# Optimization experiments

Hardware: AMD Instinct MI355X
Metric: run time of the kernel (lower is better)

## Reference

```python
import jax, jax.numpy as jnp
import numpy as np

N, E, NNZ = 50000, 10000, 250000   # nodes, hyperedges, incidences
IN_CH, H, D = 128, 64, 6           # in_channels, MLP_hidden, stalk dim
EPS = 1e-5


def setup_inputs() -> dict:
    key = jax.random.key(0)
    ks = jax.random.split(key, 12)
    inp = {}
    inp["x"] = jax.random.normal(ks[0], (N, IN_CH), jnp.float32)
    inp["hyperedge_attr"] = jax.random.normal(ks[1], (E, IN_CH), jnp.float32)  # init_hedge='rand'
    inp["node_idx"] = jax.random.randint(ks[2], (NNZ,), 0, N)
    inp["edge_idx"] = jax.random.randint(ks[3], (NNZ,), 0, E)
    inp["node_types"] = jax.random.randint(ks[4], (N,), 0, 3)
    inp["hyperedge_types"] = jax.random.randint(ks[5], (E,), 0, 6)
    s = 1.0 / np.sqrt(IN_CH)
    inp["W_lin"] = jax.random.uniform(ks[6], (IN_CH, H * D), jnp.float32, -s, s)
    inp["b_lin"] = jnp.zeros((H * D,), jnp.float32)
    inp["ln_g"] = jnp.ones((2 * H,), jnp.float32)
    inp["ln_b"] = jnp.zeros((2 * H,), jnp.float32)
    s2 = 1.0 / np.sqrt(2 * H)
    inp["W_sheaf"] = jax.random.uniform(ks[7], (2 * H, D), jnp.float32, -s2, s2)
    inp["b_sheaf"] = jnp.zeros((D,), jnp.float32)
    s3 = 1.0 / np.sqrt(H)
    inp["W_conv0"] = jax.random.uniform(ks[8], (H, H), jnp.float32, -s3, s3)
    inp["b_conv0"] = jnp.zeros((H,), jnp.float32)
    inp["W_conv1"] = jax.random.uniform(ks[9], (H, H), jnp.float32, -s3, s3)
    inp["b_conv1"] = jnp.zeros((H,), jnp.float32)
    return inp


def _layernorm(x, g, b):
    mu = x.mean(-1, keepdims=True)
    var = ((x - mu) ** 2).mean(-1, keepdims=True)
    return (x - mu) * jax.lax.rsqrt(var + EPS) * g + b


def reference(x, hyperedge_attr, node_idx, edge_idx, node_types, hyperedge_types,
              W_lin, b_lin, ln_g, ln_b, W_sheaf, b_sheaf,
              W_conv0, b_conv0, W_conv1, b_conv1):
    # --- input projection + stalk reshape (self.lin) ---
    xs = (x @ W_lin + b_lin).reshape(N * D, H)              # [N*d, H]
    es = (hyperedge_attr @ W_lin + b_lin).reshape(E * D, H)  # [E*d, H]

    # --- SheafBuilderDiag (local_concat, sigmoid act) ---
    xa = xs.reshape(N, D, H).mean(1)   # [N, H] stalk-averaged node feats
    ea = es.reshape(E, D, H).mean(1)   # [E, H]
    feat = jnp.concatenate([xa[node_idx], ea[edge_idx]], axis=-1)  # [NNZ, 2H]
    alpha = jax.nn.sigmoid(_layernorm(feat, ln_g, ln_b) @ W_sheaf + b_sheaf)  # [NNZ, D]

    dr = jnp.arange(D)
    row_exp = (node_idx[:, None] * D + dr).reshape(-1)  # [NNZ*D] expanded node index
    col_exp = (edge_idx[:, None] * D + dr).reshape(-1)  # [NNZ*D] expanded hyperedge index
    a = alpha.reshape(-1)                               # [NNZ*D]

    # --- degree_norm: D^-1 (nodes) and B^-1 (hyperedges) from incidence counts ---
    ones = jnp.ones_like(a)
    Dn = jax.ops.segment_sum(ones, row_exp, num_segments=N * D)
    Dinv = jnp.where(Dn > 0, 1.0 / Dn, 0.0)
    Bn = jax.ops.segment_sum(ones, col_exp, num_segments=E * D)
    Binv = jnp.where(Bn > 0, 1.0 / Bn, 0.0)

    def conv(xin, W, bias):
        # HyperDiffusionDiagSheafConv: out = xW - D^-1 H^T B^-1 H (xW) + bias
        xl = xin @ W
        m = Binv[:, None] * jax.ops.segment_sum(a[:, None] * xl[row_exp], col_exp, num_segments=E * D)
        agg = Dinv[:, None] * jax.ops.segment_sum(a[:, None] * m[col_exp], row_exp, num_segments=N * D)
        return xl - agg + bias

    h1 = jax.nn.elu(conv(xs, W_conv0, b_conv0))   # dropout inactive (eval)
    h2 = conv(h1, W_conv1, b_conv1)
    return jax.nn.elu(h2.reshape(N, H * D))
```

## Files before the change

### kernel.cpp

```cpp
#include <hip/hip_runtime.h>
#include <hip/hip_bf16.h>

#define N_NODES 50000
#define N_EDGES 10000
#define NNZV    250000
#define IN_CH   128
#define HDIM    64
#define DSTALK  6
#define HD      384
#define NROWS   (N_NODES * DSTALK)
#define EROWS   (N_EDGES * DSTALK)

__global__ __launch_bounds__(256) void k_wefft(
    const float* __restrict__ W_lin, const float* __restrict__ W0,
    float* __restrict__ W0effT) {
  int idx = blockIdx.x * blockDim.x + threadIdx.x;
  if (idx >= IN_CH * HD) return;
  int k = idx / HD, j = idx - k * HD;
  int r = j >> 6, h = j & 63;
  float s = 0.f;
#pragma unroll 8
  for (int m = 0; m < HDIM; m++)
    s += W_lin[k * HD + r * HDIM + m] * W0[m * HDIM + h];
  W0effT[(size_t)j * IN_CH + k] = s;
}

#define WS_BASE (IN_CH * HDIM + HD + HDIM)
#define WS_END  (WS_BASE + 780 + HDIM * HDIM)
__global__ __launch_bounds__(256) void k_wsmall(
    const float* __restrict__ W_lin, const float* __restrict__ b_lin,
    const float* __restrict__ W0, const float* __restrict__ W1,
    const float* __restrict__ g, const float* __restrict__ bln,
    const float* __restrict__ Ws, const float* __restrict__ bs,
    float* __restrict__ Wm, float* __restrict__ cm, float* __restrict__ c0,
    float* __restrict__ gwN, float* __restrict__ gwE,
    float* __restrict__ G, float* __restrict__ K, float* __restrict__ W1T) {
  int idx = blockIdx.x * blockDim.x + threadIdx.x;
  if (idx < IN_CH * HDIM) {
    int k = idx >> 6, h = idx & 63;
    float s = 0.f;
#pragma unroll
    for (int r = 0; r < DSTALK; r++) s += W_lin[k * HD + r * HDIM + h];
    Wm[idx] = s * (1.f / 6.f);
  } else if (idx < IN_CH * HDIM + HD) {
    int j = idx - IN_CH * HDIM;
    int r = j >> 6, h = j & 63;
    float s = 0.f;
#pragma unroll 8
    for (int m = 0; m < HDIM; m++) s += b_lin[r * HDIM + m] * W0[m * HDIM + h];
    c0[j] = s;
  } else if (idx < WS_BASE) {
    int h = idx - IN_CH * HDIM - HD;
    float s = 0.f;
#pragma unroll
    for (int r = 0; r < DSTALK; r++) s += b_lin[r * HDIM + h];
    cm[h] = s * (1.f / 6.f);
  } else if (idx < WS_BASE + 384) {
    int i = idx - WS_BASE;
    int h = i / 6, r = i - h * 6;
    gwN[i] = g[h] * Ws[h * DSTALK + r];
  } else if (idx < WS_BASE + 768) {
    int i = idx - WS_BASE - 384;
    int h = i / 6, r = i - h * 6;
    gwE[i] = g[64 + h] * Ws[(64 + h) * DSTALK + r];
  } else if (idx < WS_BASE + 774) {
    int r = idx - WS_BASE - 768;
    float s = 0.f;
    for (int i = 0; i < 2 * HDIM; i++) s += g[i] * Ws[i * DSTALK + r];
    G[r] = s;
  } else if (idx < WS_BASE + 780) {
    int r = idx - WS_BASE - 774;
    float s = 0.f;
    for (int i = 0; i < 2 * HDIM; i++) s += bln[i] * Ws[i * DSTALK + r];
    K[r] = s + bs[r];
  } else if (idx < WS_END) {
    int i = idx - WS_BASE - 780;
    int c = i >> 6, k = i & 63;
    W1T[c * HDIM + k] = W1[k * HDIM + c];
  }
}

__global__ __launch_bounds__(256) void k_xa_stats(
    const float* __restrict__ x, const float* __restrict__ ea,
    const float* __restrict__ Wm, const float* __restrict__ cm,
    const float* __restrict__ gwN, const float* __restrict__ gwE,
    float* __restrict__ stats) {
  __shared__ float lx[64][IN_CH];
  __shared__ float ox[64][HDIM + 1];
  __shared__ float lgw[2][64 * DSTALK];
  const int row0 = blockIdx.x * 64;
  const int tid = threadIdx.x;
  for (int i = tid; i < 2 * 64 * DSTALK; i += 256) {
    int which = i / 384, k = i - which * 384;
    lgw[which][k] = which ? gwE[k] : gwN[k];
  }
  for (int i = tid; i < 64 * IN_CH; i += 256) {
    int r = i >> 7, k = i & 127;
    int row = row0 + r;
    float v = 0.f;
    if (row < N_NODES) v = x[row * IN_CH + k];
    else if (row < N_NODES + N_EDGES) v = ea[(row - N_NODES) * IN_CH + k];
    lx[r][k] = v;
  }
  __syncthreads();
  const int col = tid & 63, rg = tid >> 6;
  float acc[16];
#pragma unroll
  for (int i = 0; i < 16; i++) acc[i] = 0.f;
  for (int k = 0; k < IN_CH; k++) {
    float w = Wm[k * HDIM + col];
#pragma unroll
    for (int i = 0; i < 16; i++) acc[i] += lx[rg * 16 + i][k] * w;
  }
  const float c = cm[col];
#pragma unroll
  for (int i = 0; i < 16; i++) ox[rg * 16 + i][col] = acc[i] + c;
  __syncthreads();
  for (int t = tid; t < 512; t += 256) {
    int row = t >> 3, st = t & 7;
    int grow = row0 + row;
    if (grow >= N_NODES + N_EDGES) continue;
    const float* __restrict__ gw = (grow >= N_NODES) ? lgw[1] : lgw[0];
    float s = 0.f;
    if (st == 0) {
#pragma unroll 8
      for (int h = 0; h < HDIM; h++) s += ox[row][h];
    } else if (st == 1) {
#pragma unroll 8
      for (int h = 0; h < HDIM; h++) { float v = ox[row][h]; s += v * v; }
    } else {
      int r = st - 2;
#pragma unroll 8
      for (int h = 0; h < HDIM; h++) s += ox[row][h] * gw[h * DSTALK + r];
    }
    stats[(size_t)grow * 8 + st] = s;
  }
}

__global__ __launch_bounds__(256, 2) void k_xl0(
    const float* __restrict__ x, const float* __restrict__ W0effT,
    const float* __restrict__ c0, float* __restrict__ xl0) {
  __shared__ float4 aS[8][129];
  __shared__ float4 bS[8][129];
  const int tid = threadIdx.x;
  const int row0 = blockIdx.x * 128;
  const int col0 = blockIdx.y * 128;
  const int tc = tid & 15, tr = tid >> 4;
  float acc[8][8];
#pragma unroll
  for (int i = 0; i < 8; i++)
#pragma unroll
    for (int j = 0; j < 8; j++) acc[i][j] = 0.f;

#pragma unroll 1
  for (int kc = 0; kc < 4; kc++) {
    if (kc) __syncthreads();
#pragma unroll
    for (int i = 0; i < 4; i++) {
      int fidx = tid + (i << 8);
      int kq = fidx & 7, row = fidx >> 3;
      int gk = kc * 32 + kq * 4;
      int grow = row0 + row;
      aS[kq][row] = (grow < N_NODES)
                        ? *(const float4*)(x + (size_t)grow * IN_CH + gk)
                        : make_float4(0.f, 0.f, 0.f, 0.f);
    }
#pragma unroll
    for (int i = 0; i < 4; i++) {
      int fidx = tid + (i << 8);
      int kq = fidx & 7, col = fidx >> 3;
      int gk = kc * 32 + kq * 4;
      bS[kq][col] =
          *(const float4*)(W0effT + (size_t)(col0 + col) * IN_CH + gk);
    }
    __syncthreads();
#pragma unroll 1
    for (int kq = 0; kq < 8; kq++) {
      float4 b[8];
#pragma unroll
      for (int j = 0; j < 8; j++) b[j] = bS[kq][tc + (j << 4)];
#pragma unroll
      for (int i = 0; i < 8; i++) {
        float4 a = aS[kq][tr + (i << 4)];
#pragma unroll
        for (int j = 0; j < 8; j++)
          acc[i][j] += a.x * b[j].x + a.y * b[j].y + a.z * b[j].z + a.w * b[j].w;
      }
    }
  }

  float cc[8];
#pragma unroll
  for (int j = 0; j < 8; j++) cc[j] = c0[col0 + tc + (j << 4)];
#pragma unroll
  for (int i = 0; i < 8; i++) {
    int row = row0 + tr + (i << 4);
    if (row >= N_NODES) continue;
    float* __restrict__ orow = xl0 + (size_t)row * HD + col0;
#pragma unroll
    for (int j = 0; j < 8; j++) {
      orow[tc + (j << 4)] = acc[i][j] + cc[j];
    }
  }
}

__global__ __launch_bounds__(256) void k_xw(
    const float* __restrict__ xin, const float* __restrict__ W1T,
    float* __restrict__ xl) {
  __shared__ float4 aS[8][129];
  __shared__ float4 bS[8][65];
  const int tid = threadIdx.x;
  const int row0 = blockIdx.x * 128;
  const int tc = tid & 15, tr = tid >> 4;
  float acc[8][4];
#pragma unroll
  for (int i = 0; i < 8; i++)
#pragma unroll
    for (int j = 0; j < 4; j++) acc[i][j] = 0.f;

#pragma unroll 1
  for (int kc = 0; kc < 2; kc++) {
    if (kc) __syncthreads();
#pragma unroll
    for (int i = 0; i < 4; i++) {
      int fidx = tid + (i << 8);
      int kq = fidx & 7, row = fidx >> 3;
      int gk = kc * 32 + kq * 4;
      int grow = row0 + row;
      aS[kq][row] = (grow < NROWS)
                        ? *(const float4*)(xin + (size_t)grow * HDIM + gk)
                        : make_float4(0.f, 0.f, 0.f, 0.f);
    }
#pragma unroll
    for (int i = 0; i < 2; i++) {
      int fidx = tid + (i << 8);
      int kq = fidx & 7, col = fidx >> 3;
      int gk = kc * 32 + kq * 4;
      bS[kq][col] = *(const float4*)(W1T + col * HDIM + gk);
    }
    __syncthreads();
#pragma unroll 1
    for (int kq = 0; kq < 8; kq++) {
      float4 b[4];
#pragma unroll
      for (int j = 0; j < 4; j++) b[j] = bS[kq][tc + (j << 4)];
#pragma unroll
      for (int i = 0; i < 8; i++) {
        float4 a = aS[kq][tr + (i << 4)];
#pragma unroll
        for (int j = 0; j < 4; j++)
          acc[i][j] += a.x * b[j].x + a.y * b[j].y + a.z * b[j].z + a.w * b[j].w;
      }
    }
  }
#pragma unroll
  for (int i = 0; i < 8; i++) {
    int row = row0 + tr + (i << 4);
    if (row >= NROWS) continue;
#pragma unroll
    for (int j = 0; j < 4; j++) {
      int col = tc + (j << 4);
      xl[(size_t)row * HDIM + col] = acc[i][j];
    }
  }
}

__global__ __launch_bounds__(256) void k_sheaf2(
    const int* __restrict__ nidx, const int* __restrict__ eidx,
    const float* __restrict__ stats,
    const float* __restrict__ G, const float* __restrict__ K,
    float* __restrict__ alpha) {
  int j = blockIdx.x * blockDim.x + threadIdx.x;
  if (j >= NNZV) return;
  int n = nidx[j], e = eidx[j];
  const float4* __restrict__ sn = (const float4*)(stats + (size_t)n * 8);
  const float4* __restrict__ se = (const float4*)(stats + ((size_t)(N_NODES + e)) * 8);
  float4 a0 = sn[0], a1 = sn[1];
  float4 b0 = se[0], b1 = se[1];
  float mu = (a0.x + b0.x) * (1.f / 128.f);
  float var = (a0.y + b0.y) * (1.f / 128.f) - mu * mu;
  float rs = rsqrtf(var + 1e-5f);
  float p[DSTALK] = {a0.z + b0.z, a0.w + b0.w, a1.x + b1.x,
                     a1.y + b1.y, a1.z + b1.z, a1.w + b1.w};
#pragma unroll
  for (int r = 0; r < DSTALK; r++) {
    float z = rs * (p[r] - mu * G[r]) + K[r];
    alpha[(size_t)j * DSTALK + r] = 1.f / (1.f + expf(-z));
  }
}

__global__ void k_count(const int* __restrict__ nidx, const int* __restrict__ eidx,
                        int* __restrict__ cntN, int* __restrict__ cntE) {
  int j = blockIdx.x * blockDim.x + threadIdx.x;
  if (j < NNZV) {
    atomicAdd(&cntN[nidx[j]], 1);
    atomicAdd(&cntE[eidx[j]], 1);
  }
}

__global__ __launch_bounds__(256) void k_scan_a(
    const int* __restrict__ cnt, int n, int* __restrict__ row,
    int* __restrict__ bsum) {
  const int b = blockIdx.x, t = threadIdx.x;
  const int i0 = b * 512 + 2 * t, i1 = i0 + 1;
  int c0 = (i0 < n) ? cnt[i0] : 0;
  int c1 = (i1 < n) ? cnt[i1] : 0;
  int ts = c0 + c1;
  const int lane = t & 63, wv = t >> 6;
  int s = ts;
#pragma unroll
  for (int o = 1; o < 64; o <<= 1) {
    int v = __shfl_up(s, o);
    if (lane >= o) s += v;
  }
  __shared__ int wsum[4];
  if (lane == 63) wsum[wv] = s;
  __syncthreads();
  int wbase = 0;
#pragma unroll
  for (int wprev = 0; wprev < 3; wprev++)
    if (wprev < wv) wbase += wsum[wprev];
  const int incl = wbase + s;
  const int excl = incl - ts;
  if (i0 < n) row[i0] = excl;
  if (i1 < n) row[i1] = excl + c0;
  if (t == 255) bsum[b] = incl;
}

__global__ __launch_bounds__(128) void k_scan_b(
    const int* __restrict__ bsum, int nb, int* __restrict__ bbase) {
  const int t = threadIdx.x;
  int v = (t < nb) ? bsum[t] : 0;
  const int lane = t & 63, wv = t >> 6;
  int s = v;
#pragma unroll
  for (int o = 1; o < 64; o <<= 1) {
    int u = __shfl_up(s, o);
    if (lane >= o) s += u;
  }
  __shared__ int wsum[2];
  if (lane == 63) wsum[wv] = s;
  __syncthreads();
  const int incl = ((wv == 1) ? wsum[0] : 0) + s;
  if (t < nb) bbase[t] = incl - v;
  if (t == 127) bbase[nb] = incl;
}

__global__ __launch_bounds__(256) void k_scan_c(
    const int* __restrict__ cnt, const int* __restrict__ bbase, int n, int nb,
    int* __restrict__ row, int* __restrict__ fill, float* __restrict__ inv) {
  int i = blockIdx.x * blockDim.x + threadIdx.x;
  if (i < n) {
    int v = row[i] + bbase[i >> 9];
    row[i] = v;
    fill[i] = v;
    int c = cnt[i];
    inv[i] = c > 0 ? 1.f / (float)c : 0.f;
  }
  if (i == 0) row[n] = bbase[nb];
}

__global__ void k_fill(const int* __restrict__ nidx, const int* __restrict__ eidx,
                       int* __restrict__ fillN, int* __restrict__ fillE,
                       int* __restrict__ jlN, int* __restrict__ jlE,
                       int* __restrict__ elN, int* __restrict__ nlE) {
  int j = blockIdx.x * blockDim.x + threadIdx.x;
  if (j < NNZV) {
    int n = nidx[j], e = eidx[j];
    int p = atomicAdd(&fillN[n], 1);
    jlN[p] = j; elN[p] = e;
    int q = atomicAdd(&fillE[e], 1);
    jlE[q] = j; nlE[q] = n;
  }
}

__global__ __launch_bounds__(256) void k_gather_e(
    const int* __restrict__ rowE, const int* __restrict__ jlE,
    const int* __restrict__ nlE, const float* __restrict__ alpha,
    const float* __restrict__ xl, const float* __restrict__ Binv,
    float* __restrict__ msum) {
  int e = (blockIdx.x * blockDim.x + threadIdx.x) >> 6;
  int lane = threadIdx.x & 63;
  if (e >= N_EDGES) return;
  float acc[DSTALK];
#pragma unroll
  for (int r = 0; r < DSTALK; r++) acc[r] = 0.f;
  const int lo = rowE[e], hi = rowE[e + 1];
  int p = lo;
  for (; p + 3 < hi; p += 4) {
    int jj[4], nn[4];
#pragma unroll
    for (int u = 0; u < 4; u++) { jj[u] = jlE[p + u]; nn[u] = nlE[p + u]; }
    float v[4][DSTALK], a[4][DSTALK];
#pragma unroll
    for (int u = 0; u < 4; u++) {
      const float* __restrict__ xr = xl + (size_t)nn[u] * HD + lane;
      const float* __restrict__ ar = alpha + (size_t)jj[u] * DSTALK;
#pragma unroll
      for (int r = 0; r < DSTALK; r++) { v[u][r] = xr[r * HDIM]; a[u][r] = ar[r]; }
    }
#pragma unroll
    for (int r = 0; r < DSTALK; r++)
      acc[r] += a[0][r] * v[0][r] + a[1][r] * v[1][r] +
                a[2][r] * v[2][r] + a[3][r] * v[3][r];
  }
  for (; p < hi; p++) {
    const int j0 = jlE[p], n0 = nlE[p];
    const float* __restrict__ xr0 = xl + (size_t)n0 * HD + lane;
    const float* __restrict__ ar0 = alpha + (size_t)j0 * DSTALK;
#pragma unroll
    for (int r = 0; r < DSTALK; r++) acc[r] += ar0[r] * xr0[r * HDIM];
  }
  const float bv = Binv[e];
  float* __restrict__ mr = msum + (size_t)e * HD + lane;
#pragma unroll
  for (int r = 0; r < DSTALK; r++) mr[r * HDIM] = acc[r] * bv;
}

__global__ __launch_bounds__(256) void k_gather_n(
    const int* __restrict__ rowN, const int* __restrict__ jlN,
    const int* __restrict__ elN, const float* __restrict__ alpha,
    const float* __restrict__ msum, const float* __restrict__ Dinv,
    const float* __restrict__ xl, const float* __restrict__ bias,
    float* __restrict__ outp) {
  int n = (blockIdx.x * blockDim.x + threadIdx.x) >> 6;
  int lane = threadIdx.x & 63;
  if (n >= N_NODES) return;
  float acc[DSTALK];
#pragma unroll
  for (int r = 0; r < DSTALK; r++) acc[r] = 0.f;
  const int lo = rowN[n], hi = rowN[n + 1];
  int p = lo;
  for (; p + 3 < hi; p += 4) {
    int jj[4], ee[4];
#pragma unroll
    for (int u = 0; u < 4; u++) { jj[u] = jlN[p + u]; ee[u] = elN[p + u]; }
    float v[4][DSTALK], a[4][DSTALK];
#pragma unroll
    for (int u = 0; u < 4; u++) {
      const float* __restrict__ mr = msum + (size_t)ee[u] * HD + lane;
      const float* __restrict__ ar = alpha + (size_t)jj[u] * DSTALK;
#pragma unroll
      for (int r = 0; r < DSTALK; r++) { v[u][r] = mr[r * HDIM]; a[u][r] = ar[r]; }
    }
#pragma unroll
    for (int r = 0; r < DSTALK; r++)
      acc[r] += a[0][r] * v[0][r] + a[1][r] * v[1][r] +
                a[2][r] * v[2][r] + a[3][r] * v[3][r];
  }
  for (; p < hi; p++) {
    const int j0 = jlN[p], e0 = elN[p];
    const float* __restrict__ mr0 = msum + (size_t)e0 * HD + lane;
    const float* __restrict__ ar0 = alpha + (size_t)j0 * DSTALK;
#pragma unroll
    for (int r = 0; r < DSTALK; r++) acc[r] += ar0[r] * mr0[r * HDIM];
  }
  const float dv = Dinv[n];
  const float bb = bias[lane];
  const float* __restrict__ xr = xl + (size_t)n * HD + lane;
  float* __restrict__ orow = outp + (size_t)n * HD + lane;
#pragma unroll
  for (int r = 0; r < DSTALK; r++) {
    float v = xr[r * HDIM] + bb - dv * acc[r];
    orow[r * HDIM] = v > 0.f ? v : expm1f(v);
  }
}

extern "C" void kernel_launch(void* const* d_in, const int* in_sizes, int n_in,
                              void* d_out, int out_size, void* d_ws, size_t ws_size,
                              hipStream_t stream) {
  const float* x    = (const float*)d_in[0];
  const float* hea  = (const float*)d_in[1];
  const int*  nidx  = (const int*)d_in[2];
  const int*  eidx  = (const int*)d_in[3];
  const float* W_lin = (const float*)d_in[6];
  const float* b_lin = (const float*)d_in[7];
  const float* ln_g  = (const float*)d_in[8];
  const float* ln_b  = (const float*)d_in[9];
  const float* W_sh  = (const float*)d_in[10];
  const float* b_sh  = (const float*)d_in[11];
  const float* W_c0  = (const float*)d_in[12];
  const float* b_c0  = (const float*)d_in[13];
  const float* W_c1  = (const float*)d_in[14];
  const float* b_c1  = (const float*)d_in[15];
  float* out = (float*)d_out;

  char* ws = (char*)d_ws;
  size_t off = 0;
  auto alloc = [&](size_t bytes) {
    size_t o = off;
    off = (off + bytes + 255) & ~(size_t)255;
    return o;
  };
  size_t o_xl0   = alloc((size_t)NROWS * HDIM * 4);
  size_t o_msum  = alloc((size_t)EROWS * HDIM * 4);
  size_t o_alpha = alloc((size_t)NNZV * DSTALK * 4);
  size_t o_stats = alloc((size_t)(N_NODES + N_EDGES) * 8 * 4);
  size_t o_jlN   = alloc((size_t)NNZV * 4);
  size_t o_jlE   = alloc((size_t)NNZV * 4);
  size_t o_elN   = alloc((size_t)NNZV * 4);
  size_t o_nlE   = alloc((size_t)NNZV * 4);
  size_t o_cntN  = alloc((size_t)N_NODES * 4);
  size_t o_cntE  = alloc((size_t)N_EDGES * 4);
  size_t o_rowN  = alloc((size_t)(N_NODES + 1) * 4);
  size_t o_rowE  = alloc((size_t)(N_EDGES + 1) * 4);
  size_t o_filN  = alloc((size_t)N_NODES * 4);
  size_t o_filE  = alloc((size_t)N_EDGES * 4);
  size_t o_Dinv  = alloc((size_t)N_NODES * 4);
  size_t o_Binv  = alloc((size_t)N_EDGES * 4);
  size_t o_bsN   = alloc((size_t)256 * 4);
  size_t o_bbN   = alloc((size_t)256 * 4);
  size_t o_bsE   = alloc((size_t)256 * 4);
  size_t o_bbE   = alloc((size_t)256 * 4);
  size_t o_WeffT = alloc((size_t)IN_CH * HD * 4);
  size_t o_Wm    = alloc((size_t)IN_CH * HDIM * 4);
  size_t o_cm    = alloc((size_t)HDIM * 4);
  size_t o_c0    = alloc((size_t)HD * 4);
  size_t o_gwN   = alloc((size_t)64 * DSTALK * 4);
  size_t o_gwE   = alloc((size_t)64 * DSTALK * 4);
  size_t o_G     = alloc((size_t)DSTALK * 4);
  size_t o_K     = alloc((size_t)DSTALK * 4);
  size_t o_W1T   = alloc((size_t)HDIM * HDIM * 4);

  float* xl0    = (float*)(ws + o_xl0);
  float* msum   = (float*)(ws + o_msum);
  float* alpha  = (float*)(ws + o_alpha);
  float* stats  = (float*)(ws + o_stats);
  int*   jlN    = (int*)(ws + o_jlN);
  int*   jlE    = (int*)(ws + o_jlE);
  int*   elN    = (int*)(ws + o_elN);
  int*   nlE    = (int*)(ws + o_nlE);
  int*   cntN   = (int*)(ws + o_cntN);
  int*   cntE   = (int*)(ws + o_cntE);
  int*   rowN   = (int*)(ws + o_rowN);
  int*   rowE   = (int*)(ws + o_rowE);
  int*   filN   = (int*)(ws + o_filN);
  int*   filE   = (int*)(ws + o_filE);
  float* Dinv   = (float*)(ws + o_Dinv);
  float* Binv   = (float*)(ws + o_Binv);
  int*   bsN    = (int*)(ws + o_bsN);
  int*   bbN    = (int*)(ws + o_bbN);
  int*   bsE    = (int*)(ws + o_bsE);
  int*   bbE    = (int*)(ws + o_bbE);
  float* W0effT = (float*)(ws + o_WeffT);
  float* Wm     = (float*)(ws + o_Wm);
  float* cm     = (float*)(ws + o_cm);
  float* c0     = (float*)(ws + o_c0);
  float* gwN    = (float*)(ws + o_gwN);
  float* gwE    = (float*)(ws + o_gwE);
  float* G      = (float*)(ws + o_G);
  float* K      = (float*)(ws + o_K);
  float* W1T    = (float*)(ws + o_W1T);

  const int NB_N = (N_NODES + 511) / 512;
  const int NB_E = (N_EDGES + 511) / 512;

  k_wefft<<<(IN_CH * HD + 255) / 256, 256, 0, stream>>>(W_lin, W_c0, W0effT);
  k_wsmall<<<(WS_END + 255) / 256, 256, 0, stream>>>(
      W_lin, b_lin, W_c0, W_c1, ln_g, ln_b, W_sh, b_sh,
      Wm, cm, c0, gwN, gwE, G, K, W1T);

  hipMemsetAsync(ws + o_cntN, 0, (size_t)N_NODES * 4, stream);
  hipMemsetAsync(ws + o_cntE, 0, (size_t)N_EDGES * 4, stream);
  k_count<<<(NNZV + 255) / 256, 256, 0, stream>>>(nidx, eidx, cntN, cntE);
  k_scan_a<<<NB_N, 256, 0, stream>>>(cntN, N_NODES, rowN, bsN);
  k_scan_a<<<NB_E, 256, 0, stream>>>(cntE, N_EDGES, rowE, bsE);
  k_scan_b<<<1, 128, 0, stream>>>(bsN, NB_N, bbN);
  k_scan_b<<<1, 128, 0, stream>>>(bsE, NB_E, bbE);
  k_scan_c<<<(N_NODES + 255) / 256, 256, 0, stream>>>(cntN, bbN, N_NODES, NB_N,
                                                      rowN, filN, Dinv);
  k_scan_c<<<(N_EDGES + 255) / 256, 256, 0, stream>>>(cntE, bbE, N_EDGES, NB_E,
                                                      rowE, filE, Binv);
  k_fill<<<(NNZV + 255) / 256, 256, 0, stream>>>(nidx, eidx, filN, filE,
                                                 jlN, jlE, elN, nlE);

  k_xa_stats<<<(N_NODES + N_EDGES + 63) / 64, 256, 0, stream>>>(
      x, hea, Wm, cm, gwN, gwE, stats);

  k_sheaf2<<<(NNZV + 255) / 256, 256, 0, stream>>>(nidx, eidx, stats, G, K, alpha);

  {
    dim3 g((N_NODES + 127) / 128, HD / 128);
    k_xl0<<<g, 256, 0, stream>>>(x, W0effT, c0, xl0);
  }
  k_gather_e<<<(N_EDGES + 3) / 4, 256, 0, stream>>>(rowE, jlE, nlE, alpha, xl0, Binv, msum);
  k_gather_n<<<(N_NODES + 3) / 4, 256, 0, stream>>>(rowN, jlN, elN, alpha, msum, Dinv,
                                                    xl0, b_c0, xl0);

  k_xw<<<(NROWS + 127) / 128, 256, 0, stream>>>(xl0, W1T, xl0);
  k_gather_e<<<(N_EDGES + 3) / 4, 256, 0, stream>>>(rowE, jlE, nlE, alpha, xl0, Binv, msum);
  k_gather_n<<<(N_NODES + 3) / 4, 256, 0, stream>>>(rowN, jlN, elN, alpha, msum, Dinv,
                                                    xl0, b_c1, out);

  (void)in_sizes; (void)n_in; (void)out_size; (void)ws_size;
}
```

Measured before the change: 653.1 us.

## Reassociate first conv edge aggregation to gather raw x then GEMM

```diff
diff --git a/kernel.cpp b/kernel.cpp
--- a/kernel.cpp
+++ b/kernel.cpp
@@ -261,6 +261,120 @@
     for (int j = 0; j < 4; j++) {
       int col = tc + (j << 4);
       xl[(size_t)row * HDIM + col] = acc[i][j];
+    }
+  }
+}
+
+__global__ __launch_bounds__(256) void k_gather_ex(
+    const int* __restrict__ rowE, const int* __restrict__ jlE,
+    const int* __restrict__ nlE, const float* __restrict__ alpha,
+    const float* __restrict__ x, const float* __restrict__ Binv,
+    float* __restrict__ ax) {
+  int e = (blockIdx.x * blockDim.x + threadIdx.x) >> 6;
+  int lane = threadIdx.x & 63;
+  if (e >= N_EDGES) return;
+  float acc0[DSTALK], acc1[DSTALK];
+#pragma unroll
+  for (int r = 0; r < DSTALK; r++) { acc0[r] = 0.f; acc1[r] = 0.f; }
+  const int lo = rowE[e], hi = rowE[e + 1];
+  int p = lo;
+  for (; p + 1 < hi; p += 2) {
+    const int j0 = jlE[p],     n0 = nlE[p];
+    const int j1 = jlE[p + 1], n1 = nlE[p + 1];
+    const float* __restrict__ xr0 = x + (size_t)n0 * IN_CH;
+    const float* __restrict__ xr1 = x + (size_t)n1 * IN_CH;
+    const float* __restrict__ ar0 = alpha + (size_t)j0 * DSTALK;
+    const float* __restrict__ ar1 = alpha + (size_t)j1 * DSTALK;
+    float x0a = xr0[lane], x0b = xr0[64 + lane];
+    float x1a = xr1[lane], x1b = xr1[64 + lane];
+    float a0[DSTALK], a1[DSTALK];
+#pragma unroll
+    for (int r = 0; r < DSTALK; r++) { a0[r] = ar0[r]; a1[r] = ar1[r]; }
+#pragma unroll
+    for (int r = 0; r < DSTALK; r++) {
+      acc0[r] += a0[r] * x0a + a1[r] * x1a;
+      acc1[r] += a0[r] * x0b + a1[r] * x1b;
+    }
+  }
+  if (p < hi) {
+    const int j0 = jlE[p], n0 = nlE[p];
+    const float* __restrict__ xr0 = x + (size_t)n0 * IN_CH;
+    const float* __restrict__ ar0 = alpha + (size_t)j0 * DSTALK;
+    float x0a = xr0[lane], x0b = xr0[64 + lane];
+#pragma unroll
+    for (int r = 0; r < DSTALK; r++) {
+      acc0[r] += ar0[r] * x0a;
+      acc1[r] += ar0[r] * x0b;
+    }
+  }
+  const float bv = Binv[e];
+  float* __restrict__ axe = ax + (size_t)e * (DSTALK * IN_CH);
+#pragma unroll
+  for (int r = 0; r < DSTALK; r++) {
+    axe[r * IN_CH + lane]      = acc0[r] * bv;
+    axe[r * IN_CH + 64 + lane] = acc1[r] * bv;
+  }
+}
+
+__global__ __launch_bounds__(256) void k_edge_gemm(
+    const float* __restrict__ ax, const float* __restrict__ W0effT,
+    float* __restrict__ msum) {
+  __shared__ float4 aS[8][129];
+  __shared__ float4 bS[8][65];
+  const int tid = threadIdx.x;
+  const int e0 = blockIdx.x * 128;
+  const int r  = blockIdx.y;
+  const int tc = tid & 15, tr = tid >> 4;
+  float acc[8][4];
+#pragma unroll
+  for (int i = 0; i < 8; i++)
+#pragma unroll
+    for (int j = 0; j < 4; j++) acc[i][j] = 0.f;
+
+#pragma unroll 1
+  for (int kc = 0; kc < 4; kc++) {
+    if (kc) __syncthreads();
+#pragma unroll
+    for (int i = 0; i < 4; i++) {
+      int fidx = tid + (i << 8);
+      int kq = fidx & 7, row = fidx >> 3;
+      int gk = kc * 32 + kq * 4;
+      int ge = e0 + row;
+      aS[kq][row] = (ge < N_EDGES)
+          ? *(const float4*)(ax + ((size_t)ge * DSTALK + r) * IN_CH + gk)
+          : make_float4(0.f, 0.f, 0.f, 0.f);
+    }
+#pragma unroll
+    for (int i = 0; i < 2; i++) {
+      int fidx = tid + (i << 8);
+      int kq = fidx & 7, col = fidx >> 3;
+      int gk = kc * 32 + kq * 4;
+      bS[kq][col] =
+          *(const float4*)(W0effT + (size_t)(r * 64 + col) * IN_CH + gk);
+    }
+    __syncthreads();
+#pragma unroll 1
+    for (int kq = 0; kq < 8; kq++) {
+      float4 b[4];
+#pragma unroll
+      for (int j = 0; j < 4; j++) b[j] = bS[kq][tc + (j << 4)];
+#pragma unroll
+      for (int i = 0; i < 8; i++) {
+        float4 a = aS[kq][tr + (i << 4)];
+#pragma unroll
+        for (int j = 0; j < 4; j++)
+          acc[i][j] += a.x * b[j].x + a.y * b[j].y + a.z * b[j].z + a.w * b[j].w;
+      }
+    }
+  }
+#pragma unroll
+  for (int i = 0; i < 8; i++) {
+    int ge = e0 + tr + (i << 4);
+    if (ge >= N_EDGES) continue;
+    float* __restrict__ mrow = msum + (size_t)ge * HD + r * 64;
+#pragma unroll
+    for (int j = 0; j < 4; j++) {
+      mrow[tc + (j << 4)] = acc[i][j];
     }
   }
 }
@@ -552,6 +666,8 @@
   float* K      = (float*)(ws + o_K);
   float* W1T    = (float*)(ws + o_W1T);
 
+  float* ax = (float*)d_out;
+
   const int NB_N = (N_NODES + 511) / 512;
   const int NB_E = (N_EDGES + 511) / 512;
 
@@ -579,11 +695,16 @@
 
   k_sheaf2<<<(NNZV + 255) / 256, 256, 0, stream>>>(nidx, eidx, stats, G, K, alpha);
 
+  k_gather_ex<<<(N_EDGES + 3) / 4, 256, 0, stream>>>(rowE, jlE, nlE, alpha, x,
+                                                     Binv, ax);
+  {
+    dim3 ge((N_EDGES + 127) / 128, DSTALK);
+    k_edge_gemm<<<ge, 256, 0, stream>>>(ax, W0effT, msum);
+  }
   {
     dim3 g((N_NODES + 127) / 128, HD / 128);
     k_xl0<<<g, 256, 0, stream>>>(x, W0effT, c0, xl0);
   }
-  k_gather_e<<<(N_EDGES + 3) / 4, 256, 0, stream>>>(rowE, jlE, nlE, alpha, xl0, Binv, msum);
   k_gather_n<<<(N_NODES + 3) / 4, 256, 0, stream>>>(rowN, jlN, elN, alpha, msum, Dinv,
                                                     xl0, b_c0, xl0);
 
```

New measurement: 652.6 us. No clear change (-0.1%).
